# Optimization experiments

Measured on AMD Instinct MI355X. Metric: run time of the kernel, lower is better.

Reference implementation:

```python
import jax, jax.numpy as jnp
import numpy as np

INPUT_DIM = 2048
OUTPUT_DIM = 16000
BATCH = 512


def _make_sketch(key, input_dim, output_dim):
    kh, ks = jax.random.split(key)
    rand_h = jax.random.randint(kh, (input_dim,), 0, output_dim)
    rand_s = (2 * jax.random.randint(ks, (input_dim,), 0, 2) - 1).astype(jnp.float32)
    # count-sketch matrix: one signed nonzero per row (duplicates sum, matching
    # torch.sparse .to_dense())
    return jnp.zeros((input_dim, output_dim), jnp.float32).at[jnp.arange(input_dim), rand_h].add(rand_s)


def setup_inputs() -> dict:
    key = jax.random.key(0)
    k1, k2, k3, k4 = jax.random.split(key, 4)
    return {
        "x1": jax.random.normal(k1, (BATCH, INPUT_DIM), jnp.float32),
        "x2": jax.random.normal(k2, (BATCH, INPUT_DIM), jnp.float32),
        "sketch1": _make_sketch(k3, INPUT_DIM, OUTPUT_DIM),
        "sketch2": _make_sketch(k4, INPUT_DIM, OUTPUT_DIM),
    }


def reference(x1, x2, sketch1, sketch2):
    d = sketch1.shape[1]  # output_dim
    # count-sketch projection (dense GEMM, as in the original)
    p1 = x1 @ sketch1  # [B, D]
    p2 = x2 @ sketch2  # [B, D]
    # circular convolution via FFT
    f1 = jnp.fft.rfft(p1, axis=-1)
    f2 = jnp.fft.rfft(p2, axis=-1)
    # torch.irfft (old API) did NOT normalize -> equals numpy irfft * D; the
    # module then multiplies by output_dim again, matching `* self.output_dim`.
    cbp = jnp.fft.irfft(f1 * f2, n=d, axis=-1) * d
    # signed square root
    ss = jnp.sqrt(jax.nn.relu(cbp)) - jnp.sqrt(jax.nn.relu(-cbp))
    # L2 normalize along dim=0 (the batch dim, as written in the original)
    norm = jnp.sqrt(jnp.sum(ss * ss, axis=0, keepdims=True))
    return ss / jnp.maximum(norm, 1e-12)
```

## Files before the change

kernel.cpp:

```cpp
#include <hip/hip_runtime.h>
#include <math.h>

#define D_OUT 16000
#define IN_DIM 2048
#define BATCH 512
#define T2 1024
#define PAD 129

__device__ __forceinline__ float2 cmul(float2 a, float2 b) {
    return make_float2(a.x * b.x - a.y * b.y, a.x * b.y + a.y * b.x);
}
__device__ __forceinline__ float2 cadd(float2 a, float2 b) { return make_float2(a.x + b.x, a.y + b.y); }
__device__ __forceinline__ float2 csub(float2 a, float2 b) { return make_float2(a.x - b.x, a.y - b.y); }

__device__ __forceinline__ int PZ(int j, int i) { return j * PAD + i; }

template<int INV>
__device__ __forceinline__ float2 ctw(float2 w) { if (INV) w.y = -w.y; return w; }

__device__ __forceinline__ int div125(int m) { return (int)(((unsigned)m * 33555u) >> 22); }

template<int INV>
__device__ __forceinline__ float2 bigtw(int m, const float2* w128f, const float2* wNf) {
    int a = div125(m);
    int b = m - a * 125;
    float2 r = cmul(w128f[a], wNf[b]);
    if (INV) r.y = -r.y;
    return r;
}

template<int INV>
__device__ __forceinline__ void dft5(float2& b0, float2& b1, float2& b2, float2& b3, float2& b4) {
    const float C1 = 0.30901699437494742f, S1 = 0.95105651629515357f;
    const float C2 = -0.80901699437494745f, S2 = 0.58778525229247314f;
    float2 t1 = cadd(b1, b4), t2 = csub(b1, b4);
    float2 t3 = cadd(b2, b3), t4 = csub(b2, b3);
    float2 X0 = make_float2(b0.x + t1.x + t3.x, b0.y + t1.y + t3.y);
    float2 m1 = make_float2(b0.x + C1 * t1.x + C2 * t3.x, b0.y + C1 * t1.y + C2 * t3.y);
    float2 m2 = make_float2(b0.x + C2 * t1.x + C1 * t3.x, b0.y + C2 * t1.y + C1 * t3.y);
    float2 n1 = make_float2(S1 * t2.x + S2 * t4.x, S1 * t2.y + S2 * t4.y);
    float2 n2 = make_float2(S2 * t2.x - S1 * t4.x, S2 * t2.y - S1 * t4.y);
    if (!INV) {
        b1 = make_float2(m1.x + n1.y, m1.y - n1.x);
        b4 = make_float2(m1.x - n1.y, m1.y + n1.x);
        b2 = make_float2(m2.x + n2.y, m2.y - n2.x);
        b3 = make_float2(m2.x - n2.y, m2.y + n2.x);
    } else {
        b1 = make_float2(m1.x - n1.y, m1.y + n1.x);
        b4 = make_float2(m1.x + n1.y, m1.y - n1.x);
        b2 = make_float2(m2.x - n2.y, m2.y + n2.x);
        b3 = make_float2(m2.x + n2.y, m2.y - n2.x);
    }
    b0 = X0;
}

__global__ void extract_kernel(const float* __restrict__ sk1, const float* __restrict__ sk2,
                               int* __restrict__ h1, float* __restrict__ s1,
                               int* __restrict__ h2, float* __restrict__ s2) {
    int row = blockIdx.x & (IN_DIM - 1);
    bool second = blockIdx.x >= IN_DIM;
    const float* sk = second ? sk2 : sk1;
    const float4* base = (const float4*)(sk + (size_t)row * D_OUT);
    float hacc = 0.f, sacc = 0.f;
    for (int j = threadIdx.x; j < D_OUT / 4; j += 256) {
        float4 v = base[j];
        float j4 = (float)(4 * j);
        hacc += j4 * fabsf(v.x) + (j4 + 1.f) * fabsf(v.y) +
                (j4 + 2.f) * fabsf(v.z) + (j4 + 3.f) * fabsf(v.w);
        sacc += v.x + v.y + v.z + v.w;
    }
    for (int off = 32; off; off >>= 1) {
        hacc += __shfl_down(hacc, off);
        sacc += __shfl_down(sacc, off);
    }
    __shared__ float sh[8];
    int lane = threadIdx.x & 63, wv = threadIdx.x >> 6;
    if (lane == 0) { sh[wv] = hacc; sh[wv + 4] = sacc; }
    __syncthreads();
    if (threadIdx.x == 0) {
        float h = sh[0] + sh[1] + sh[2] + sh[3];
        float s = sh[4] + sh[5] + sh[6] + sh[7];
        int* hh = second ? h2 : h1;
        float* ss = second ? s2 : s1;
        hh[row] = (int)(h + 0.5f);
        ss[row] = s;
    }
}

__global__ void __launch_bounds__(T2, 1) cbp_kernel(
    const float* __restrict__ x1, const float* __restrict__ x2,
    const int* __restrict__ h1, const float* __restrict__ s1,
    const int* __restrict__ h2, const float* __restrict__ s2,
    float* __restrict__ out) {
    __shared__ float2 smem[125 * PAD + 125 + 128 + 125];
    float2* z = smem;
    float2* w125 = smem + 125 * PAD;
    float2* w128f = w125 + 125;
    float2* wNf = w128f + 128;
    const int tid = threadIdx.x;
    const int b = blockIdx.x;

    for (int t = tid; t < 125; t += T2) {
        float s, c;
        sincospif(t * (2.0f / 125.0f), &s, &c);
        w125[t] = make_float2(c, -s);
        sincospif(t * (1.0f / 8000.0f), &s, &c);
        wNf[t] = make_float2(c, -s);
    }
    for (int a = tid; a < 128; a += T2) {
        float s, c;
        sincospif(a * (1.0f / 64.0f), &s, &c);
        w128f[a] = make_float2(c, -s);
    }
    for (int i = tid; i < 125 * PAD; i += T2) z[i] = make_float2(0.f, 0.f);
    __syncthreads();

    const float* x1r = x1 + (size_t)b * IN_DIM;
    const float* x2r = x2 + (size_t)b * IN_DIM;
    float* zf = (float*)z;
    for (int i = tid; i < IN_DIM; i += T2) {
        int n1 = h1[i] >> 7, n2 = h1[i] & 127;
        int jr = 25 * (n1 % 5) + 5 * ((n1 / 5) % 5) + n1 / 25;
        atomicAdd(&zf[2 * PZ(jr, n2)], x1r[i] * s1[i]);
        n1 = h2[i] >> 7; n2 = h2[i] & 127;
        jr = 25 * (n1 % 5) + 5 * ((n1 / 5) % 5) + n1 / 25;
        atomicAdd(&zf[2 * PZ(jr, n2) + 1], x2r[i] * s2[i]);
    }
    __syncthreads();

    for (int w = tid; w < 3200; w += T2) {
        int i = w & 127, g = w >> 7;
        int p = PZ(5 * g, i);
        float2 b0 = z[p], b1 = z[p + PAD], b2 = z[p + 2 * PAD], b3 = z[p + 3 * PAD], b4 = z[p + 4 * PAD];
        dft5<0>(b0, b1, b2, b3, b4);
        z[p] = b0; z[p + PAD] = b1; z[p + 2 * PAD] = b2; z[p + 3 * PAD] = b3; z[p + 4 * PAD] = b4;
    }
    __syncthreads();
    for (int w = tid; w < 3200; w += T2) {
        int i = w & 127, j5 = w >> 7;
        int g = j5 / 5, q = j5 - 5 * g;
        int p = PZ(g * 25 + q, i);
        float2 b0 = z[p];
        float2 b1 = cmul(z[p + 5 * PAD], w125[q * 5]);
        float2 b2 = cmul(z[p + 10 * PAD], w125[q * 10]);
        float2 b3 = cmul(z[p + 15 * PAD], w125[q * 15]);
        float2 b4 = cmul(z[p + 20 * PAD], w125[q * 20]);
        dft5<0>(b0, b1, b2, b3, b4);
        z[p] = b0; z[p + 5 * PAD] = b1; z[p + 10 * PAD] = b2; z[p + 15 * PAD] = b3; z[p + 20 * PAD] = b4;
    }
    __syncthreads();
    for (int w = tid; w < 3200; w += T2) {
        int i = w & 127, q = w >> 7;
        int p = PZ(q, i);
        float2 b0 = z[p];
        float2 b1 = cmul(z[p + 25 * PAD], w125[q]);
        float2 b2 = cmul(z[p + 50 * PAD], w125[q * 2]);
        float2 b3 = cmul(z[p + 75 * PAD], w125[q * 3]);
        float2 b4 = cmul(z[p + 100 * PAD], w125[q * 4]);
        dft5<0>(b0, b1, b2, b3, b4);
        z[p]             = cmul(b0, bigtw<0>(i * q, w128f, wNf));
        z[p + 25 * PAD]  = cmul(b1, bigtw<0>(i * (q + 25), w128f, wNf));
        z[p + 50 * PAD]  = cmul(b2, bigtw<0>(i * (q + 50), w128f, wNf));
        z[p + 75 * PAD]  = cmul(b3, bigtw<0>(i * (q + 75), w128f, wNf));
        z[p + 100 * PAD] = cmul(b4, bigtw<0>(i * (q + 100), w128f, wNf));
    }
    __syncthreads();

    for (int idx = tid; idx < 2000; idx += T2) {
        int q = idx / 125, j = idx - q * 125;
        int p0 = PZ(j, q);
        float2 x[8];
#pragma unroll
        for (int t = 0; t < 8; t++) x[t] = z[p0 + 16 * t];
#pragma unroll
        for (int t = 0; t < 4; t++) {
            float2 u = cadd(x[t], x[t + 4]);
            float2 d = csub(x[t], x[t + 4]);
            x[t + 4] = cmul(d, w128f[q + 16 * t]);
            x[t] = u;
        }
        {
            float2 wA = w128f[2 * q], wB = w128f[2 * q + 32];
            float2 u, d;
            u = cadd(x[0], x[2]); d = csub(x[0], x[2]); x[0] = u; x[2] = cmul(d, wA);
            u = cadd(x[1], x[3]); d = csub(x[1], x[3]); x[1] = u; x[3] = cmul(d, wB);
            u = cadd(x[4], x[6]); d = csub(x[4], x[6]); x[4] = u; x[6] = cmul(d, wA);
            u = cadd(x[5], x[7]); d = csub(x[5], x[7]); x[5] = u; x[7] = cmul(d, wB);
        }
        {
            float2 wC = w128f[4 * q];
#pragma unroll
            for (int s = 0; s < 4; s++) {
                float2 u = cadd(x[2 * s], x[2 * s + 1]);
                float2 d = csub(x[2 * s], x[2 * s + 1]);
                x[2 * s] = u; x[2 * s + 1] = cmul(d, wC);
            }
        }
#pragma unroll
        for (int t = 0; t < 8; t++) z[p0 + 16 * t] = x[t];
    }
    __syncthreads();
    for (int idx = tid; idx < 4000; idx += T2) {
        int m = idx / 125, j = idx - m * 125;
        int c = m & 3, g = m >> 2;
        int p = PZ(j, 16 * g + c);
        float2 x0 = z[p], x1 = z[p + 4], x2 = z[p + 8], x3 = z[p + 12];
        float2 wA = w128f[8 * c], wB = w128f[8 * c + 32], wC = w128f[16 * c];
        float2 u, d;
        u = cadd(x0, x2); d = csub(x0, x2); x0 = u; x2 = cmul(d, wA);
        u = cadd(x1, x3); d = csub(x1, x3); x1 = u; x3 = cmul(d, wB);
        u = cadd(x0, x1); d = csub(x0, x1); x0 = u; x1 = cmul(d, wC);
        u = cadd(x2, x3); d = csub(x2, x3); x2 = u; x3 = cmul(d, wC);
        z[p] = x0; z[p + 4] = x1; z[p + 8] = x2; z[p + 12] = x3;
    }
    __syncthreads();
    for (int idx = tid; idx < 4000; idx += T2) {
        int g = idx / 125, j = idx - g * 125;
        int p = PZ(j, 4 * g);
        float2 x0 = z[p], x1 = z[p + 1], x2 = z[p + 2], x3 = z[p + 3];
        float2 u0 = cadd(x0, x2), v0 = csub(x0, x2);
        float2 u1 = cadd(x1, x3), dd = csub(x1, x3);
        float2 v1 = make_float2(dd.y, -dd.x);
        z[p]     = cadd(u0, u1);
        z[p + 1] = csub(u0, u1);
        z[p + 2] = cadd(v0, v1);
        z[p + 3] = csub(v0, v1);
    }
    __syncthreads();

    for (int k = tid; k <= 8000; k += T2) {
        int k1 = k % 125, k2 = k / 125;
        int km = (k == 0) ? 0 : 16000 - k;
        int k1m = km % 125, k2m = km / 125;
        int p = PZ(k1, __brev((unsigned)k2) >> 25);
        int pm = PZ(k1m, __brev((unsigned)k2m) >> 25);
        float2 Zk = z[p], Zm = z[pm];
        float2 F1 = make_float2(0.5f * (Zk.x + Zm.x), 0.5f * (Zk.y - Zm.y));
        float2 F2 = make_float2(0.5f * (Zk.y + Zm.y), -0.5f * (Zk.x - Zm.x));
        float2 G = cmul(F1, F2);
        z[p] = G;
        z[pm] = make_float2(G.x, -G.y);
    }
    __syncthreads();

    for (int idx = tid; idx < 4000; idx += T2) {
        int g = idx / 125, j = idx - g * 125;
        int p = PZ(j, 4 * g);
        float2 x0 = z[p], x1 = z[p + 1], x2 = z[p + 2], x3 = z[p + 3];
        float2 a0 = cadd(x0, x1), a1 = csub(x0, x1);
        float2 a2 = cadd(x2, x3), a3 = csub(x2, x3);
        float2 w3 = make_float2(-a3.y, a3.x);
        z[p]     = cadd(a0, a2);
        z[p + 1] = cadd(a1, w3);
        z[p + 2] = csub(a0, a2);
        z[p + 3] = csub(a1, w3);
    }
    __syncthreads();
    for (int idx = tid; idx < 4000; idx += T2) {
        int m = idx / 125, j = idx - m * 125;
        int q = m & 3, g = m >> 2;
        int p = PZ(j, 16 * g + q);
        float2 xa = z[p], xb = z[p + 4], xc = z[p + 8], xd = z[p + 12];
        float2 w8 = ctw<1>(w128f[q * 16]);
        float2 t = cmul(w8, xb);
        float2 a = cadd(xa, t), bb = csub(xa, t);
        t = cmul(w8, xd);
        float2 c = cadd(xc, t), d = csub(xc, t);
        float2 w16a = ctw<1>(w128f[q * 8]);
        float2 w16b = ctw<1>(w128f[(q + 4) * 8]);
        t = cmul(w16a, c); z[p] = cadd(a, t);      z[p + 8]  = csub(a, t);
        t = cmul(w16b, d); z[p + 4] = cadd(bb, t); z[p + 12] = csub(bb, t);
    }
    __syncthreads();
    for (int idx = tid; idx < 2000; idx += T2) {
        int q = idx / 125, j = idx - q * 125;
        int p0 = PZ(j, q);
        float2 x[8];
#pragma unroll
        for (int t = 0; t < 8; t++) x[t] = z[p0 + 16 * t];
        float2 w = ctw<1>(w128f[q * 4]);
#pragma unroll
        for (int s = 0; s < 4; s++) {
            float2 t = cmul(w, x[2 * s + 1]);
            x[2 * s + 1] = csub(x[2 * s], t);
            x[2 * s]     = cadd(x[2 * s], t);
        }
        float2 wA = ctw<1>(w128f[q * 2]);
        float2 wB = ctw<1>(w128f[q * 2 + 32]);
        {
            float2 t = cmul(wA, x[2]); x[2] = csub(x[0], t); x[0] = cadd(x[0], t);
            t = cmul(wB, x[3]); x[3] = csub(x[1], t); x[1] = cadd(x[1], t);
            t = cmul(wA, x[6]); x[6] = csub(x[4], t); x[4] = cadd(x[4], t);
            t = cmul(wB, x[7]); x[7] = csub(x[5], t); x[5] = cadd(x[5], t);
        }
#pragma unroll
        for (int t = 0; t < 4; t++) {
            float2 wv = ctw<1>(w128f[q + 16 * t]);
            float2 tt = cmul(wv, x[t + 4]);
            x[t + 4] = csub(x[t], tt);
            x[t]     = cadd(x[t], tt);
        }
#pragma unroll
        for (int t = 0; t < 8; t++)
            z[p0 + 16 * t] = cmul(x[t], bigtw<1>((q + 16 * t) * j, w128f, wNf));
    }
    __syncthreads();

    for (int w = tid; w < 3200; w += T2) {
        int i = w & 127, q = w >> 7;
        int p = PZ(q, i);
        float2 b0 = z[p], b1 = z[p + 25 * PAD], b2 = z[p + 50 * PAD],
               b3 = z[p + 75 * PAD], b4 = z[p + 100 * PAD];
        dft5<1>(b0, b1, b2, b3, b4);
        z[p]             = b0;
        z[p + 25 * PAD]  = cmul(b1, ctw<1>(w125[q]));
        z[p + 50 * PAD]  = cmul(b2, ctw<1>(w125[2 * q]));
        z[p + 75 * PAD]  = cmul(b3, ctw<1>(w125[3 * q]));
        z[p + 100 * PAD] = cmul(b4, ctw<1>(w125[4 * q]));
    }
    __syncthreads();
    for (int w = tid; w < 3200; w += T2) {
        int i = w & 127, j5 = w >> 7;
        int u1 = j5 / 5, q2 = j5 - 5 * u1;
        int p = PZ(25 * u1 + q2, i);
        float2 b0 = z[p], b1 = z[p + 5 * PAD], b2 = z[p + 10 * PAD],
               b3 = z[p + 15 * PAD], b4 = z[p + 20 * PAD];
        dft5<1>(b0, b1, b2, b3, b4);
        z[p]            = b0;
        z[p + 5 * PAD]  = cmul(b1, ctw<1>(w125[5 * q2]));
        z[p + 10 * PAD] = cmul(b2, ctw<1>(w125[10 * q2]));
        z[p + 15 * PAD] = cmul(b3, ctw<1>(w125[15 * q2]));
        z[p + 20 * PAD] = cmul(b4, ctw<1>(w125[20 * q2]));
    }
    __syncthreads();
    float* orow = out + (size_t)b * D_OUT;
    for (int w = tid; w < 3200; w += T2) {
        int i = w & 127, g = w >> 7;
        int p = PZ(5 * g, i);
        float2 b0 = z[p], b1 = z[p + PAD], b2 = z[p + 2 * PAD],
               b3 = z[p + 3 * PAD], b4 = z[p + 4 * PAD];
        dft5<1>(b0, b1, b2, b3, b4);
        int nbase = 5 * (g % 5) + g / 25 + (g / 5) % 5 * 0;
        int g5 = g % 5, gd = g / 5;
        float re[5] = { b0.x, b1.x, b2.x, b3.x, b4.x };
#pragma unroll
        for (int u = 0; u < 5; u++) {
            int n1 = 25 * u + 5 * g5 + gd;
            float c = re[u];
            orow[n1 * 128 + i] = (c > 0.f) ? sqrtf(c) : -sqrtf(-c);
        }
        (void)nbase;
    }
}

__global__ void colsum_kernel(const float* __restrict__ out, float* __restrict__ colsum) {
    __shared__ float sm[512];
    int c = threadIdx.x & 63, r = threadIdx.x >> 6;
    int col = blockIdx.x * 64 + c;
    float acc = 0.f;
    for (int row = r; row < BATCH; row += 8) {
        float v = out[(size_t)row * D_OUT + col];
        acc += v * v;
    }
    sm[threadIdx.x] = acc;
    __syncthreads();
    if (r == 0) {
        float s = sm[c] + sm[c + 64] + sm[c + 128] + sm[c + 192] +
                  sm[c + 256] + sm[c + 320] + sm[c + 384] + sm[c + 448];
        colsum[col] = s;
    }
}

__global__ void normalize_kernel(float* __restrict__ out, const float* __restrict__ colsum) {
    int idx = blockIdx.x * 256 + threadIdx.x;
    float4* o4 = (float4*)out;
    float4 v = o4[idx];
    int n = (idx * 4) % D_OUT;
    const float4 cs = *(const float4*)(colsum + n);
    v.x /= fmaxf(sqrtf(cs.x), 1e-12f);
    v.y /= fmaxf(sqrtf(cs.y), 1e-12f);
    v.z /= fmaxf(sqrtf(cs.z), 1e-12f);
    v.w /= fmaxf(sqrtf(cs.w), 1e-12f);
    o4[idx] = v;
}

extern "C" void kernel_launch(void* const* d_in, const int* in_sizes, int n_in,
                              void* d_out, int out_size, void* d_ws, size_t ws_size,
                              hipStream_t stream) {
    (void)in_sizes; (void)n_in; (void)out_size; (void)ws_size;
    const float* x1 = (const float*)d_in[0];
    const float* x2 = (const float*)d_in[1];
    const float* sk1 = (const float*)d_in[2];
    const float* sk2 = (const float*)d_in[3];
    float* out = (float*)d_out;

    char* ws = (char*)d_ws;
    int* h1 = (int*)(ws);
    float* s1 = (float*)(ws + 8192);
    int* h2 = (int*)(ws + 16384);
    float* s2 = (float*)(ws + 24576);
    float* colsum = (float*)(ws + 32768);

    extract_kernel<<<2 * IN_DIM, 256, 0, stream>>>(sk1, sk2, h1, s1, h2, s2);
    cbp_kernel<<<BATCH, T2, 0, stream>>>(x1, x2, h1, s1, h2, s2, out);
    colsum_kernel<<<250, 512, 0, stream>>>(out, colsum);
    normalize_kernel<<<8000, 256, 0, stream>>>(out, colsum);
}
```

Measured before the change: 393.9 us.

## Restructure 128-point FFT into radix-16x8 passes and widen sketch extraction

The forward and inverse 128-point FFT stages are regrouped from three passes (radix-8, radix-4, radix-4) into two passes (radix-16 over stride 8, then radix-8 over contiguous elements). This cuts the number of block-wide barriers and shared-memory round trips per batch row. The sketch extraction kernel now uses 512 threads, each issuing eight independent float4 loads up front to raise memory-level parallelism, and the shared buffer is zeroed with float4 stores. The cost is higher register pressure from the 16-element arrays, and only 1000 of the 1024 threads do work in the radix-16 passes.

```diff
diff --git a/kernel.cpp b/kernel.cpp
--- a/kernel.cpp
+++ b/kernel.cpp
@@ -61,25 +61,32 @@
     bool second = blockIdx.x >= IN_DIM;
     const float* sk = second ? sk2 : sk1;
     const float4* base = (const float4*)(sk + (size_t)row * D_OUT);
+    const int t = threadIdx.x;
     float hacc = 0.f, sacc = 0.f;
-    for (int j = threadIdx.x; j < D_OUT / 4; j += 256) {
-        float4 v = base[j];
-        float j4 = (float)(4 * j);
-        hacc += j4 * fabsf(v.x) + (j4 + 1.f) * fabsf(v.y) +
-                (j4 + 2.f) * fabsf(v.z) + (j4 + 3.f) * fabsf(v.w);
-        sacc += v.x + v.y + v.z + v.w;
+    if (t < 500) {
+        float4 v[8];
+#pragma unroll
+        for (int c = 0; c < 8; c++) v[c] = base[t + 500 * c];
+#pragma unroll
+        for (int c = 0; c < 8; c++) {
+            float j4 = (float)(4 * (t + 500 * c));
+            hacc += j4 * fabsf(v[c].x) + (j4 + 1.f) * fabsf(v[c].y) +
+                    (j4 + 2.f) * fabsf(v[c].z) + (j4 + 3.f) * fabsf(v[c].w);
+            sacc += v[c].x + v[c].y + v[c].z + v[c].w;
+        }
     }
     for (int off = 32; off; off >>= 1) {
         hacc += __shfl_down(hacc, off);
         sacc += __shfl_down(sacc, off);
     }
-    __shared__ float sh[8];
-    int lane = threadIdx.x & 63, wv = threadIdx.x >> 6;
-    if (lane == 0) { sh[wv] = hacc; sh[wv + 4] = sacc; }
-    __syncthreads();
-    if (threadIdx.x == 0) {
-        float h = sh[0] + sh[1] + sh[2] + sh[3];
-        float s = sh[4] + sh[5] + sh[6] + sh[7];
+    __shared__ float sh[16];
+    int lane = t & 63, wv = t >> 6;
+    if (lane == 0) { sh[wv] = hacc; sh[wv + 8] = sacc; }
+    __syncthreads();
+    if (t == 0) {
+        float h = 0.f, s = 0.f;
+#pragma unroll
+        for (int w = 0; w < 8; w++) { h += sh[w]; s += sh[w + 8]; }
         int* hh = second ? h2 : h1;
         float* ss = second ? s2 : s1;
         hh[row] = (int)(h + 0.5f);
@@ -92,9 +99,9 @@
     const int* __restrict__ h1, const float* __restrict__ s1,
     const int* __restrict__ h2, const float* __restrict__ s2,
     float* __restrict__ out) {
-    __shared__ float2 smem[125 * PAD + 125 + 128 + 125];
+    __shared__ float2 smem[125 * PAD + 1 + 125 + 128 + 125];
     float2* z = smem;
-    float2* w125 = smem + 125 * PAD;
+    float2* w125 = smem + 125 * PAD + 1;
     float2* w128f = w125 + 125;
     float2* wNf = w128f + 128;
     const int tid = threadIdx.x;
@@ -112,7 +119,10 @@
         sincospif(a * (1.0f / 64.0f), &s, &c);
         w128f[a] = make_float2(c, -s);
     }
-    for (int i = tid; i < 125 * PAD; i += T2) z[i] = make_float2(0.f, 0.f);
+    {
+        float4* z4 = (float4*)z;
+        for (int i = tid; i < 8063; i += T2) z4[i] = make_float4(0.f, 0.f, 0.f, 0.f);
+    }
     __syncthreads();
 
     const float* x1r = x1 + (size_t)b * IN_DIM;
@@ -166,65 +176,80 @@
     }
     __syncthreads();
 
+    if (tid < 1000) {
+        int q = tid / 125, j = tid - q * 125;
+        int p = PZ(j, q);
+        float2 x[16];
+#pragma unroll
+        for (int t = 0; t < 16; t++) x[t] = z[p + 8 * t];
+#pragma unroll
+        for (int t = 0; t < 8; t++) {
+            float2 u = cadd(x[t], x[t + 8]);
+            float2 d = csub(x[t], x[t + 8]);
+            x[t + 8] = cmul(d, w128f[q + 8 * t]);
+            x[t] = u;
+        }
+#pragma unroll
+        for (int h = 0; h < 16; h += 8)
+            for (int t = h; t < h + 4; t++) {
+                float2 u = cadd(x[t], x[t + 4]);
+                float2 d = csub(x[t], x[t + 4]);
+                x[t + 4] = cmul(d, w128f[2 * q + 16 * (t & 7)]);
+                x[t] = u;
+            }
+#pragma unroll
+        for (int h = 0; h < 16; h += 4)
+            for (int t = h; t < h + 2; t++) {
+                float2 u = cadd(x[t], x[t + 2]);
+                float2 d = csub(x[t], x[t + 2]);
+                x[t + 2] = cmul(d, w128f[4 * q + 32 * (t & 3)]);
+                x[t] = u;
+            }
+        {
+            float2 w16 = w128f[8 * q];
+#pragma unroll
+            for (int t = 0; t < 16; t += 2) {
+                float2 u = cadd(x[t], x[t + 1]);
+                float2 d = csub(x[t], x[t + 1]);
+                x[t + 1] = cmul(d, w16);
+                x[t] = u;
+            }
+        }
+#pragma unroll
+        for (int t = 0; t < 16; t++) z[p + 8 * t] = x[t];
+    }
+    __syncthreads();
     for (int idx = tid; idx < 2000; idx += T2) {
-        int q = idx / 125, j = idx - q * 125;
-        int p0 = PZ(j, q);
+        int g = idx / 125, j = idx - g * 125;
+        int p = PZ(j, 8 * g);
         float2 x[8];
 #pragma unroll
-        for (int t = 0; t < 8; t++) x[t] = z[p0 + 16 * t];
-#pragma unroll
-        for (int t = 0; t < 4; t++) {
-            float2 u = cadd(x[t], x[t + 4]);
-            float2 d = csub(x[t], x[t + 4]);
-            x[t + 4] = cmul(d, w128f[q + 16 * t]);
-            x[t] = u;
-        }
-        {
-            float2 wA = w128f[2 * q], wB = w128f[2 * q + 32];
-            float2 u, d;
-            u = cadd(x[0], x[2]); d = csub(x[0], x[2]); x[0] = u; x[2] = cmul(d, wA);
-            u = cadd(x[1], x[3]); d = csub(x[1], x[3]); x[1] = u; x[3] = cmul(d, wB);
-            u = cadd(x[4], x[6]); d = csub(x[4], x[6]); x[4] = u; x[6] = cmul(d, wA);
-            u = cadd(x[5], x[7]); d = csub(x[5], x[7]); x[5] = u; x[7] = cmul(d, wB);
-        }
-        {
-            float2 wC = w128f[4 * q];
-#pragma unroll
-            for (int s = 0; s < 4; s++) {
-                float2 u = cadd(x[2 * s], x[2 * s + 1]);
-                float2 d = csub(x[2 * s], x[2 * s + 1]);
-                x[2 * s] = u; x[2 * s + 1] = cmul(d, wC);
-            }
-        }
-#pragma unroll
-        for (int t = 0; t < 8; t++) z[p0 + 16 * t] = x[t];
-    }
-    __syncthreads();
-    for (int idx = tid; idx < 4000; idx += T2) {
-        int m = idx / 125, j = idx - m * 125;
-        int c = m & 3, g = m >> 2;
-        int p = PZ(j, 16 * g + c);
-        float2 x0 = z[p], x1 = z[p + 4], x2 = z[p + 8], x3 = z[p + 12];
-        float2 wA = w128f[8 * c], wB = w128f[8 * c + 32], wC = w128f[16 * c];
-        float2 u, d;
-        u = cadd(x0, x2); d = csub(x0, x2); x0 = u; x2 = cmul(d, wA);
-        u = cadd(x1, x3); d = csub(x1, x3); x1 = u; x3 = cmul(d, wB);
-        u = cadd(x0, x1); d = csub(x0, x1); x0 = u; x1 = cmul(d, wC);
-        u = cadd(x2, x3); d = csub(x2, x3); x2 = u; x3 = cmul(d, wC);
-        z[p] = x0; z[p + 4] = x1; z[p + 8] = x2; z[p + 12] = x3;
-    }
-    __syncthreads();
-    for (int idx = tid; idx < 4000; idx += T2) {
-        int g = idx / 125, j = idx - g * 125;
-        int p = PZ(j, 4 * g);
-        float2 x0 = z[p], x1 = z[p + 1], x2 = z[p + 2], x3 = z[p + 3];
-        float2 u0 = cadd(x0, x2), v0 = csub(x0, x2);
-        float2 u1 = cadd(x1, x3), dd = csub(x1, x3);
-        float2 v1 = make_float2(dd.y, -dd.x);
-        z[p]     = cadd(u0, u1);
-        z[p + 1] = csub(u0, u1);
-        z[p + 2] = cadd(v0, v1);
-        z[p + 3] = csub(v0, v1);
+        for (int d = 0; d < 8; d++) x[d] = z[p + d];
+#pragma unroll
+        for (int d = 0; d < 4; d++) {
+            float2 u = cadd(x[d], x[d + 4]);
+            float2 v = csub(x[d], x[d + 4]);
+            x[d + 4] = cmul(v, w128f[16 * d]);
+            x[d] = u;
+        }
+#pragma unroll
+        for (int h = 0; h < 8; h += 4) {
+            float2 u = cadd(x[h], x[h + 2]);
+            float2 v = csub(x[h], x[h + 2]);
+            x[h] = u; x[h + 2] = v;
+            u = cadd(x[h + 1], x[h + 3]);
+            v = csub(x[h + 1], x[h + 3]);
+            x[h + 1] = u;
+            x[h + 3] = make_float2(v.y, -v.x);
+        }
+#pragma unroll
+        for (int d = 0; d < 8; d += 2) {
+            float2 u = cadd(x[d], x[d + 1]);
+            float2 v = csub(x[d], x[d + 1]);
+            x[d] = u; x[d + 1] = v;
+        }
+#pragma unroll
+        for (int d = 0; d < 8; d++) z[p + d] = x[d];
     }
     __syncthreads();
 
@@ -243,66 +268,79 @@
     }
     __syncthreads();
 
-    for (int idx = tid; idx < 4000; idx += T2) {
+    for (int idx = tid; idx < 2000; idx += T2) {
         int g = idx / 125, j = idx - g * 125;
-        int p = PZ(j, 4 * g);
-        float2 x0 = z[p], x1 = z[p + 1], x2 = z[p + 2], x3 = z[p + 3];
-        float2 a0 = cadd(x0, x1), a1 = csub(x0, x1);
-        float2 a2 = cadd(x2, x3), a3 = csub(x2, x3);
-        float2 w3 = make_float2(-a3.y, a3.x);
-        z[p]     = cadd(a0, a2);
-        z[p + 1] = cadd(a1, w3);
-        z[p + 2] = csub(a0, a2);
-        z[p + 3] = csub(a1, w3);
-    }
-    __syncthreads();
-    for (int idx = tid; idx < 4000; idx += T2) {
-        int m = idx / 125, j = idx - m * 125;
-        int q = m & 3, g = m >> 2;
-        int p = PZ(j, 16 * g + q);
-        float2 xa = z[p], xb = z[p + 4], xc = z[p + 8], xd = z[p + 12];
-        float2 w8 = ctw<1>(w128f[q * 16]);
-        float2 t = cmul(w8, xb);
-        float2 a = cadd(xa, t), bb = csub(xa, t);
-        t = cmul(w8, xd);
-        float2 c = cadd(xc, t), d = csub(xc, t);
-        float2 w16a = ctw<1>(w128f[q * 8]);
-        float2 w16b = ctw<1>(w128f[(q + 4) * 8]);
-        t = cmul(w16a, c); z[p] = cadd(a, t);      z[p + 8]  = csub(a, t);
-        t = cmul(w16b, d); z[p + 4] = cadd(bb, t); z[p + 12] = csub(bb, t);
-    }
-    __syncthreads();
-    for (int idx = tid; idx < 2000; idx += T2) {
-        int q = idx / 125, j = idx - q * 125;
-        int p0 = PZ(j, q);
+        int p = PZ(j, 8 * g);
         float2 x[8];
 #pragma unroll
-        for (int t = 0; t < 8; t++) x[t] = z[p0 + 16 * t];
-        float2 w = ctw<1>(w128f[q * 4]);
-#pragma unroll
-        for (int s = 0; s < 4; s++) {
-            float2 t = cmul(w, x[2 * s + 1]);
-            x[2 * s + 1] = csub(x[2 * s], t);
-            x[2 * s]     = cadd(x[2 * s], t);
-        }
-        float2 wA = ctw<1>(w128f[q * 2]);
-        float2 wB = ctw<1>(w128f[q * 2 + 32]);
+        for (int d = 0; d < 8; d++) x[d] = z[p + d];
+#pragma unroll
+        for (int d = 0; d < 8; d += 2) {
+            float2 t = x[d + 1];
+            x[d + 1] = csub(x[d], t);
+            x[d] = cadd(x[d], t);
+        }
+#pragma unroll
+        for (int h = 0; h < 8; h += 4) {
+            float2 t = x[h + 2];
+            x[h + 2] = csub(x[h], t);
+            x[h] = cadd(x[h], t);
+            float2 s = x[h + 3];
+            t = make_float2(-s.y, s.x);
+            x[h + 3] = csub(x[h + 1], t);
+            x[h + 1] = cadd(x[h + 1], t);
+        }
+#pragma unroll
+        for (int d = 0; d < 4; d++) {
+            float2 t = cmul(ctw<1>(w128f[16 * d]), x[d + 4]);
+            x[d + 4] = csub(x[d], t);
+            x[d] = cadd(x[d], t);
+        }
+#pragma unroll
+        for (int d = 0; d < 8; d++) z[p + d] = x[d];
+    }
+    __syncthreads();
+    if (tid < 1000) {
+        int q = tid / 125, j = tid - q * 125;
+        int p = PZ(j, q);
+        float2 x[16];
+#pragma unroll
+        for (int t = 0; t < 16; t++) x[t] = z[p + 8 * t];
         {
-            float2 t = cmul(wA, x[2]); x[2] = csub(x[0], t); x[0] = cadd(x[0], t);
-            t = cmul(wB, x[3]); x[3] = csub(x[1], t); x[1] = cadd(x[1], t);
-            t = cmul(wA, x[6]); x[6] = csub(x[4], t); x[4] = cadd(x[4], t);
-            t = cmul(wB, x[7]); x[7] = csub(x[5], t); x[5] = cadd(x[5], t);
-        }
-#pragma unroll
-        for (int t = 0; t < 4; t++) {
-            float2 wv = ctw<1>(w128f[q + 16 * t]);
-            float2 tt = cmul(wv, x[t + 4]);
-            x[t + 4] = csub(x[t], tt);
-            x[t]     = cadd(x[t], tt);
-        }
-#pragma unroll
-        for (int t = 0; t < 8; t++)
-            z[p0 + 16 * t] = cmul(x[t], bigtw<1>((q + 16 * t) * j, w128f, wNf));
+            float2 w16 = ctw<1>(w128f[8 * q]);
+#pragma unroll
+            for (int t = 0; t < 16; t += 2) {
+                float2 tt = cmul(w16, x[t + 1]);
+                x[t + 1] = csub(x[t], tt);
+                x[t] = cadd(x[t], tt);
+            }
+        }
+#pragma unroll
+        for (int h = 0; h < 16; h += 4)
+            for (int t = h; t < h + 2; t++) {
+                float2 w = ctw<1>(w128f[4 * q + 32 * (t & 3)]);
+                float2 tt = cmul(w, x[t + 2]);
+                x[t + 2] = csub(x[t], tt);
+                x[t] = cadd(x[t], tt);
+            }
+#pragma unroll
+        for (int h = 0; h < 16; h += 8)
+            for (int t = h; t < h + 4; t++) {
+                float2 w = ctw<1>(w128f[2 * q + 16 * (t & 7)]);
+                float2 tt = cmul(w, x[t + 4]);
+                x[t + 4] = csub(x[t], tt);
+                x[t] = cadd(x[t], tt);
+            }
+#pragma unroll
+        for (int t = 0; t < 8; t++) {
+            float2 w = ctw<1>(w128f[q + 8 * t]);
+            float2 tt = cmul(w, x[t + 8]);
+            x[t + 8] = csub(x[t], tt);
+            x[t] = cadd(x[t], tt);
+        }
+#pragma unroll
+        for (int t = 0; t < 16; t++)
+            z[p + 8 * t] = cmul(x[t], bigtw<1>((q + 8 * t) * j, w128f, wNf));
     }
     __syncthreads();
 
@@ -340,7 +378,6 @@
         float2 b0 = z[p], b1 = z[p + PAD], b2 = z[p + 2 * PAD],
                b3 = z[p + 3 * PAD], b4 = z[p + 4 * PAD];
         dft5<1>(b0, b1, b2, b3, b4);
-        int nbase = 5 * (g % 5) + g / 25 + (g / 5) % 5 * 0;
         int g5 = g % 5, gd = g / 5;
         float re[5] = { b0.x, b1.x, b2.x, b3.x, b4.x };
 #pragma unroll
@@ -349,7 +386,6 @@
             float c = re[u];
             orow[n1 * 128 + i] = (c > 0.f) ? sqrtf(c) : -sqrtf(-c);
         }
-        (void)nbase;
     }
 }
 
@@ -401,7 +437,7 @@
     float* s2 = (float*)(ws + 24576);
     float* colsum = (float*)(ws + 32768);
 
-    extract_kernel<<<2 * IN_DIM, 256, 0, stream>>>(sk1, sk2, h1, s1, h2, s2);
+    extract_kernel<<<2 * IN_DIM, 512, 0, stream>>>(sk1, sk2, h1, s1, h2, s2);
     cbp_kernel<<<BATCH, T2, 0, stream>>>(x1, x2, h1, s1, h2, s2, out);
     colsum_kernel<<<250, 512, 0, stream>>>(out, colsum);
     normalize_kernel<<<8000, 256, 0, stream>>>(out, colsum);
```

Result: faster. 385.0 us (-2.3%).
